# Kernel tuning notes

Measured on AMD Instinct MI355X. Metric: run time of the kernel, lower is better.

Reference implementation:

```python
import jax, jax.numpy as jnp
import numpy as np

B, C, H, W = 4, 128, 256, 256
HIDDEN = max(C // 8, 4)  # SE hidden


def haar_dwt(x):
    # x: (B,C,H,W), H,W even. Haar 2x2 stride-2 depthwise conv via block reshape.
    b_, c_, h_, w_ = x.shape
    xb = x.reshape(b_, c_, h_ // 2, 2, w_ // 2, 2)
    a = xb[:, :, :, 0, :, 0]
    b = xb[:, :, :, 0, :, 1]
    c = xb[:, :, :, 1, :, 0]
    d = xb[:, :, :, 1, :, 1]
    LL = 0.5 * (a + b + c + d)
    LH = 0.5 * (-a + b - c + d)
    HL = 0.5 * (-a - b + c + d)
    HH = 0.5 * (a - b - c + d)
    return LH, HL, HH, LL


def haar_idwt(LH, HL, HH, LL):
    # inverse of the depthwise conv_transpose with the same Haar kernels
    a = 0.5 * (LL - LH - HL + HH)
    b = 0.5 * (LL + LH - HL - HH)
    c = 0.5 * (LL - LH + HL - HH)
    d = 0.5 * (LL + LH + HL + HH)
    top = jnp.stack([a, b], axis=-1)      # (B,C,h,w,2)
    bot = jnp.stack([c, d], axis=-1)      # (B,C,h,w,2)
    blk = jnp.stack([top, bot], axis=-2)  # (B,C,h,w,2,2) -> rows x cols
    Bs, Cs, h, w = LL.shape
    return blk.transpose(0, 1, 2, 4, 3, 5).reshape(Bs, Cs, 2 * h, 2 * w)


def soft_threshold(x, thr):
    return jnp.sign(x) * jax.nn.relu(jnp.abs(x) - thr)


def setup_inputs() -> dict:
    key = jax.random.key(0)
    ks = jax.random.split(key, 9)
    x = jax.random.normal(ks[0], (B, C, H, W), dtype=jnp.float32)
    theta = jax.random.normal(ks[1], (3, C, 1, 1), dtype=jnp.float32) * 0.02
    dir_gate = jax.random.normal(ks[2], (3, C, 1, 1), dtype=jnp.float32) * 0.02
    fc_w = jax.random.normal(ks[3], (C, C), dtype=jnp.float32) * (1.0 / np.sqrt(C))
    fc_b = jax.random.normal(ks[4], (C,), dtype=jnp.float32) * 0.02
    sub_redistribute = jax.random.normal(ks[5], (C, 3), dtype=jnp.float32) * 0.02
    se_w1 = jax.random.normal(ks[6], (HIDDEN, C), dtype=jnp.float32) * (1.0 / np.sqrt(C))
    se_b1 = jnp.zeros((HIDDEN,), dtype=jnp.float32)
    se_w2 = jax.random.normal(ks[7], (C, HIDDEN), dtype=jnp.float32) * (1.0 / np.sqrt(HIDDEN))
    se_b2 = jnp.zeros((C,), dtype=jnp.float32)
    gamma = jnp.float32(0.5)
    return {"x": x, "theta": theta, "dir_gate": dir_gate, "fc_w": fc_w,
            "fc_b": fc_b, "sub_redistribute": sub_redistribute,
            "se_w1": se_w1, "se_b1": se_b1, "se_w2": se_w2, "se_b2": se_b2,
            "gamma": gamma}


def reference(x, theta, dir_gate, fc_w, fc_b, sub_redistribute,
              se_w1, se_b1, se_w2, se_b2, gamma):
    eps = 1e-6
    LH, HL, HH, LL = haar_dwt(x)

    # per-(B,C) abs-mean thresholds
    m_LH = jnp.mean(jnp.abs(LH), axis=(2, 3), keepdims=True) + eps
    m_HL = jnp.mean(jnp.abs(HL), axis=(2, 3), keepdims=True) + eps
    m_HH = jnp.mean(jnp.abs(HH), axis=(2, 3), keepdims=True) + eps
    t = jax.nn.sigmoid(theta)  # (3,C,1,1)
    LH_hat = soft_threshold(LH, t[0][None] * m_LH)
    HL_hat = soft_threshold(HL, t[1][None] * m_HL)
    HH_hat = soft_threshold(HH, t[2][None] * m_HH)

    g = jax.nn.sigmoid(dir_gate)
    LH_hat = LH_hat * g[0][None]
    HL_hat = HL_hat * g[1][None]
    HH_hat = HH_hat * g[2][None]

    stack3 = jnp.stack([LH_hat, HL_hat, HH_hat], axis=2)  # (B,C,3,h,w)
    attn_band = jax.nn.softmax(jnp.mean(jnp.abs(stack3), axis=1, keepdims=True), axis=2)
    H_mix = jnp.sum(stack3 * attn_band, axis=2)  # (B,C,h,w)

    w_redis = jax.nn.softmax(sub_redistribute, axis=1)  # (C,3)
    H_redist = H_mix[:, :, None] * w_redis[None, :, :, None, None]  # (B,C,3,h,w)
    X_re = haar_idwt(H_redist[:, :, 0], H_redist[:, :, 1], H_redist[:, :, 2], LL)

    # channel softmax gate from GAP + fc
    gap_vec = jnp.mean(X_re, axis=(2, 3))  # (B,C)
    gap_vec = gap_vec @ fc_w.T + fc_b
    w_softmax = jax.nn.softmax(gap_vec, axis=1)[:, :, None, None]

    # SE gate
    z = jnp.mean(X_re, axis=(2, 3))  # (B,C)
    z = jax.nn.relu(z @ se_w1.T + se_b1)
    w_se = jax.nn.sigmoid(z @ se_w2.T + se_b2)[:, :, None, None]

    return x * w_softmax + gamma * (X_re * w_se)
```

## Files before the change

### kernel.cpp

```cpp
#include <hip/hip_runtime.h>
#include <math.h>

#define BB 4
#define CC 128
#define HHH 256
#define WWW 256
#define HWSZ (HHH*WWW)
#define HIDDEN 16
#define NPAIR 8192
#define FCHUNK 16
#define NFCHUNK (NPAIR/FCHUNK)
#define RQUART 4

typedef float nfloat4 __attribute__((ext_vector_type(4)));

struct CParams {
    float thr0, thr1, thr2;
    float gA0, gA1, gA2;
    float gF0, gF1, gF2;
    float wsm, e0q;
    float ca, cb, cc, cd;
    float pad0;
};
static_assert(sizeof(CParams) == 64, "CParams must be 64B");

__device__ __forceinline__ float sigmoidf_(float v) { return 1.0f / (1.0f + expf(-v)); }

__global__ __launch_bounds__(256) void k_reduce(const float* __restrict__ x,
                                                float4* __restrict__ partial) {
    const int bq = blockIdx.x;
    const int bc = bq >> 2;
    const int quarter = bq & 3;
    const float* base = x + (size_t)bc * HWSZ;
    const int tid = threadIdx.x;
    float a0 = 0.f, a1 = 0.f, a2 = 0.f, sx = 0.f;
    #pragma unroll
    for (int i = 0; i < 8; ++i) {
        const int p = quarter * 2048 + i * 256 + tid;
        const int r = p >> 6;
        const int q = p & 63;
        const float4 t  = *(const float4*)(base + (2*r)   * WWW + 4*q);
        const float4 bo = *(const float4*)(base + (2*r+1) * WWW + 4*q);
        {   const float a = t.x, b_ = t.y, c_ = bo.x, d = bo.y;
            const float u1 = a + b_, u2 = c_ + d, u3 = a + c_, u4 = b_ + d, u5 = a + d, u6 = b_ + c_;
            a0 += fabsf(u4 - u3);
            a1 += fabsf(u2 - u1);
            a2 += fabsf(u5 - u6);
            sx += u1 + u2;
        }
        {   const float a = t.z, b_ = t.w, c_ = bo.z, d = bo.w;
            const float u1 = a + b_, u2 = c_ + d, u3 = a + c_, u4 = b_ + d, u5 = a + d, u6 = b_ + c_;
            a0 += fabsf(u4 - u3);
            a1 += fabsf(u2 - u1);
            a2 += fabsf(u5 - u6);
            sx += u1 + u2;
        }
    }
    __shared__ float4 red[256];
    red[tid] = make_float4(a0, a1, a2, sx);
    __syncthreads();
    for (int off = 128; off > 0; off >>= 1) {
        if (tid < off) {
            float4 o = red[tid + off];
            red[tid].x += o.x; red[tid].y += o.y; red[tid].z += o.z; red[tid].w += o.w;
        }
        __syncthreads();
    }
    if (tid == 0) partial[bq] = red[0];
}

__global__ __launch_bounds__(128) void k_params(
    const float4* __restrict__ partial,
    const float* __restrict__ theta, const float* __restrict__ dir_gate,
    const float* __restrict__ fc_w, const float* __restrict__ fc_b,
    const float* __restrict__ sub_r,
    const float* __restrict__ se_w1, const float* __restrict__ se_b1,
    const float* __restrict__ se_w2, const float* __restrict__ se_b2,
    const float* __restrict__ gamma_p,
    CParams* __restrict__ cbuf)
{
    const int b = blockIdx.x;
    const int i = threadIdx.x;
    __shared__ float gap[CC];
    __shared__ float z1[HIDDEN];
    __shared__ float red[CC];

    float4 s = make_float4(0.f, 0.f, 0.f, 0.f);
    #pragma unroll
    for (int k = 0; k < RQUART; ++k) {
        const float4 pq = partial[(b * CC + i) * RQUART + k];
        s.x += pq.x; s.y += pq.y; s.z += pq.z; s.w += pq.w;
    }
    gap[i] = s.w * (1.0f / 65536.0f);
    __syncthreads();

    float y = fc_b[i];
    for (int j = 0; j < CC; ++j) y += gap[j] * fc_w[i * CC + j];
    if (i < HIDDEN) {
        float z = se_b1[i];
        for (int j = 0; j < CC; ++j) z += gap[j] * se_w1[i * CC + j];
        z1[i] = fmaxf(z, 0.0f);
    }
    red[i] = y;
    __syncthreads();
    float mx = -1e30f;
    for (int j = 0; j < CC; ++j) mx = fmaxf(mx, red[j]);
    const float e = expf(y - mx);
    __syncthreads();
    red[i] = e;
    __syncthreads();
    float ssum = 0.f;
    for (int j = 0; j < CC; ++j) ssum += red[j];
    const float wsm = e / ssum;

    float wse = se_b2[i];
    for (int h = 0; h < HIDDEN; ++h) wse += z1[h] * se_w2[i * HIDDEN + h];
    wse = sigmoidf_(wse);
    const float wse2 = gamma_p[0] * wse;

    const float m0 = s.x * (0.5f / 16384.0f) + 1e-6f;
    const float m1 = s.y * (0.5f / 16384.0f) + 1e-6f;
    const float m2 = s.z * (0.5f / 16384.0f) + 1e-6f;
    CParams p;
    const float g0 = sigmoidf_(dir_gate[0 * CC + i]);
    const float g1 = sigmoidf_(dir_gate[1 * CC + i]);
    const float g2 = sigmoidf_(dir_gate[2 * CC + i]);
    p.thr0 = 2.0f * sigmoidf_(theta[0 * CC + i]) * m0;
    p.thr1 = 2.0f * sigmoidf_(theta[1 * CC + i]) * m1;
    p.thr2 = 2.0f * sigmoidf_(theta[2 * CC + i]) * m2;
    p.gA0 = g0; p.gA1 = g1; p.gA2 = g2;
    p.gF0 = 0.5f * g0 * wse2;
    p.gF1 = 0.5f * g1 * wse2;
    p.gF2 = 0.5f * g2 * wse2;
    p.wsm = wsm;
    p.e0q = 0.25f * wse2;
    const float r0 = sub_r[i * 3 + 0], r1 = sub_r[i * 3 + 1], r2 = sub_r[i * 3 + 2];
    const float rm = fmaxf(r0, fmaxf(r1, r2));
    const float e0 = expf(r0 - rm), e1 = expf(r1 - rm), e2 = expf(r2 - rm);
    const float inv = 1.0f / (e0 + e1 + e2);
    const float w0 = e0 * inv, w1 = e1 * inv, w2 = e2 * inv;
    p.ca = 0.5f * (-w0 - w1 + w2);
    p.cb = 0.5f * ( w0 - w1 - w2);
    p.cc = 0.5f * (-w0 + w1 - w2);
    p.cd = 0.5f * ( w0 + w1 + w2);
    p.pad0 = 0.f;
    cbuf[b * CC + i] = p;
}

__global__ __launch_bounds__(256) void k_fused(const float* __restrict__ x,
                                               const CParams* __restrict__ cbuf,
                                               float* __restrict__ out) {
    const int b = blockIdx.y;
    const int chunk = blockIdx.x;
    const int tid = threadIdx.x;
    const int pp = tid & 15;
    const int g  = tid >> 4;

    __shared__ CParams cp[CC];
    __shared__ float red2[16][16][6];
    __shared__ float att2[16][4];
    {
        const float* src = (const float*)(cbuf + b * CC);
        float* dst = (float*)cp;
        for (int i = tid; i < CC * 16; i += 256) dst[i] = src[i];
    }
    __syncthreads();

    const int p  = chunk * FCHUNK + pp;
    const int rp = p >> 6, q = p & 63;
    const float* base = x + (size_t)b * CC * HWSZ + (2*rp) * WWW + 4*q;

    float4 st[8], sb[8];
    float sA0=0, sA1=0, sA2=0, sB0=0, sB1=0, sB2=0;
    #pragma unroll
    for (int ci = 0; ci < 8; ++ci) {
        const int c = g * 8 + ci;
        const float* pc = base + c * HWSZ;
        st[ci] = *(const float4*)(pc);
        sb[ci] = *(const float4*)(pc + WWW);
        const float thr0 = cp[c].thr0, thr1 = cp[c].thr1, thr2 = cp[c].thr2;
        const float gA0 = cp[c].gA0, gA1 = cp[c].gA1, gA2 = cp[c].gA2;
        {   const float a = st[ci].x, b_ = st[ci].y, c_ = sb[ci].x, d = sb[ci].y;
            const float u1 = a + b_, u2 = c_ + d, u3 = a + c_, u4 = b_ + d, u5 = a + d, u6 = b_ + c_;
            sA0 += gA0 * fmaxf(fabsf(u4 - u3) - thr0, 0.f);
            sA1 += gA1 * fmaxf(fabsf(u2 - u1) - thr1, 0.f);
            sA2 += gA2 * fmaxf(fabsf(u5 - u6) - thr2, 0.f);
        }
        {   const float a = st[ci].z, b_ = st[ci].w, c_ = sb[ci].z, d = sb[ci].w;
            const float u1 = a + b_, u2 = c_ + d, u3 = a + c_, u4 = b_ + d, u5 = a + d, u6 = b_ + c_;
            sB0 += gA0 * fmaxf(fabsf(u4 - u3) - thr0, 0.f);
            sB1 += gA1 * fmaxf(fabsf(u2 - u1) - thr1, 0.f);
            sB2 += gA2 * fmaxf(fabsf(u5 - u6) - thr2, 0.f);
        }
    }
    red2[g][pp][0] = sA0; red2[g][pp][1] = sA1; red2[g][pp][2] = sA2;
    red2[g][pp][3] = sB0; red2[g][pp][4] = sB1; red2[g][pp][5] = sB2;
    __syncthreads();

    if (tid < 32) {
        const int pair = tid >> 1, h = tid & 1;
        float v0 = 0.f, v1 = 0.f, v2 = 0.f;
        #pragma unroll
        for (int gg = 0; gg < 16; ++gg) {
            v0 += red2[gg][pair][3*h + 0];
            v1 += red2[gg][pair][3*h + 1];
            v2 += red2[gg][pair][3*h + 2];
        }
        v0 *= (0.5f / CC); v1 *= (0.5f / CC); v2 *= (0.5f / CC);
        const float mx = fmaxf(v0, fmaxf(v1, v2));
        const float e0 = expf(v0 - mx), e1 = expf(v1 - mx), e2 = expf(v2 - mx);
        const float inv = 1.0f / (e0 + e1 + e2);
        att2[pair][2*h + 0] = e0 * inv;
        att2[pair][2*h + 1] = e1 * inv;
    }
    __syncthreads();

    const float a0A = att2[pp][0], a1A = att2[pp][1], a2A = 1.0f - a0A - a1A;
    const float a0B = att2[pp][2], a1B = att2[pp][3], a2B = 1.0f - a0B - a1B;

    float* obase = out + (size_t)b * CC * HWSZ + (2*rp) * WWW + 4*q;
    #pragma unroll
    for (int ci = 0; ci < 8; ++ci) {
        const int c = g * 8 + ci;
        const float thr0 = cp[c].thr0, thr1 = cp[c].thr1, thr2 = cp[c].thr2;
        const float gF0 = cp[c].gF0, gF1 = cp[c].gF1, gF2 = cp[c].gF2;
        const float wsm = cp[c].wsm, e0q = cp[c].e0q;
        const float ca = cp[c].ca, cb = cp[c].cb, ccc = cp[c].cc, cd = cp[c].cd;
        const float m0A = a0A * gF0, m1A = a1A * gF1, m2A = a2A * gF2;
        const float m0B = a0B * gF0, m1B = a1B * gF1, m2B = a2B * gF2;
        nfloat4 otop, obot;
        {   const float a = st[ci].x, b_ = st[ci].y, c_ = sb[ci].x, d = sb[ci].y;
            const float u1 = a + b_, u2 = c_ + d, u3 = a + c_, u4 = b_ + d, u5 = a + d, u6 = b_ + c_;
            const float B0 = u4 - u3, B1 = u2 - u1, B2 = u5 - u6;
            const float LL2 = u1 + u2;
            const float s0 = copysignf(fmaxf(fabsf(B0) - thr0, 0.f), B0);
            const float s1 = copysignf(fmaxf(fabsf(B1) - thr1, 0.f), B1);
            const float s2 = copysignf(fmaxf(fabsf(B2) - thr2, 0.f), B2);
            const float Hf = s0*m0A + s1*m1A + s2*m2A;
            const float T  = e0q * LL2;
            otop.x = fmaf(a , wsm, fmaf(Hf, ca , T));
            otop.y = fmaf(b_, wsm, fmaf(Hf, cb , T));
            obot.x = fmaf(c_, wsm, fmaf(Hf, ccc, T));
            obot.y = fmaf(d , wsm, fmaf(Hf, cd , T));
        }
        {   const float a = st[ci].z, b_ = st[ci].w, c_ = sb[ci].z, d = sb[ci].w;
            const float u1 = a + b_, u2 = c_ + d, u3 = a + c_, u4 = b_ + d, u5 = a + d, u6 = b_ + c_;
            const float B0 = u4 - u3, B1 = u2 - u1, B2 = u5 - u6;
            const float LL2 = u1 + u2;
            const float s0 = copysignf(fmaxf(fabsf(B0) - thr0, 0.f), B0);
            const float s1 = copysignf(fmaxf(fabsf(B1) - thr1, 0.f), B1);
            const float s2 = copysignf(fmaxf(fabsf(B2) - thr2, 0.f), B2);
            const float Hf = s0*m0B + s1*m1B + s2*m2B;
            const float T  = e0q * LL2;
            otop.z = fmaf(a , wsm, fmaf(Hf, ca , T));
            otop.w = fmaf(b_, wsm, fmaf(Hf, cb , T));
            obot.z = fmaf(c_, wsm, fmaf(Hf, ccc, T));
            obot.w = fmaf(d , wsm, fmaf(Hf, cd , T));
        }
        float* po = obase + c * HWSZ;
        __builtin_nontemporal_store(otop, (nfloat4*)(po));
        __builtin_nontemporal_store(obot, (nfloat4*)(po + WWW));
    }
}

extern "C" void kernel_launch(void* const* d_in, const int* in_sizes, int n_in,
                              void* d_out, int out_size, void* d_ws, size_t ws_size,
                              hipStream_t stream) {
    const float* x        = (const float*)d_in[0];
    const float* theta    = (const float*)d_in[1];
    const float* dir_gate = (const float*)d_in[2];
    const float* fc_w     = (const float*)d_in[3];
    const float* fc_b     = (const float*)d_in[4];
    const float* sub_r    = (const float*)d_in[5];
    const float* se_w1    = (const float*)d_in[6];
    const float* se_b1    = (const float*)d_in[7];
    const float* se_w2    = (const float*)d_in[8];
    const float* se_b2    = (const float*)d_in[9];
    const float* gamma_p  = (const float*)d_in[10];
    float* out = (float*)d_out;

    char* ws = (char*)d_ws;
    float4*  partial = (float4*)(ws);
    CParams* cbuf    = (CParams*)(ws + 32768);

    k_reduce<<<dim3(BB * CC * RQUART), dim3(256), 0, stream>>>(x, partial);
    k_params<<<dim3(BB), dim3(CC), 0, stream>>>(partial, theta, dir_gate, fc_w, fc_b,
                                                sub_r, se_w1, se_b1, se_w2, se_b2,
                                                gamma_p, cbuf);
    k_fused<<<dim3(NFCHUNK, BB), dim3(256), 0, stream>>>(x, cbuf, out);
}
```

Before: 75.36 us.

## Halve pixels per block, 4 channels per thread, pad channel params in LDS

The fused kernel now handles 8 pixel pairs per block instead of 16, with 32 channel groups of 4 channels each instead of 16 groups of 8. This halves the number of float4 values each thread keeps live across the band-attention reduction, which should lower register pressure and raise occupancy, and it doubles the grid size. The per-channel parameter table in shared memory is padded to a stride of 17 floats to avoid LDS bank conflicts. The cross-group reduction becomes a two-stage shared-memory reduction with an extra barrier. The cost is more blocks, each reloading the parameter table, and more reduction traffic.

```diff
diff --git a/kernel.cpp b/kernel.cpp
--- a/kernel.cpp
+++ b/kernel.cpp
@@ -8,9 +8,11 @@
 #define HWSZ (HHH*WWW)
 #define HIDDEN 16
 #define NPAIR 8192
-#define FCHUNK 16
-#define NFCHUNK (NPAIR/FCHUNK)
+#define FP 8
+#define NFCHUNK (NPAIR/FP)
+#define NG 32
 #define RQUART 4
+#define CPW 17
 
 typedef float nfloat4 __attribute__((ext_vector_type(4)));
 
@@ -153,33 +155,37 @@
     const int b = blockIdx.y;
     const int chunk = blockIdx.x;
     const int tid = threadIdx.x;
-    const int pp = tid & 15;
-    const int g  = tid >> 4;
-
-    __shared__ CParams cp[CC];
-    __shared__ float red2[16][16][6];
-    __shared__ float att2[16][4];
+    const int pp = tid & 7;
+    const int g  = tid >> 3;
+
+    __shared__ float cpa[CC * CPW];
+    __shared__ float red2[NG][FP][6];
+    __shared__ float vsum[FP][6];
+    __shared__ float att2[FP][4];
     {
         const float* src = (const float*)(cbuf + b * CC);
-        float* dst = (float*)cp;
-        for (int i = tid; i < CC * 16; i += 256) dst[i] = src[i];
-    }
-    __syncthreads();
-
-    const int p  = chunk * FCHUNK + pp;
+        for (int i = tid; i < CC * 16; i += 256) {
+            const int c = i >> 4, f = i & 15;
+            cpa[c * CPW + f] = src[i];
+        }
+    }
+    __syncthreads();
+
+    const int p  = chunk * FP + pp;
     const int rp = p >> 6, q = p & 63;
     const float* base = x + (size_t)b * CC * HWSZ + (2*rp) * WWW + 4*q;
 
-    float4 st[8], sb[8];
+    float4 st[4], sb[4];
     float sA0=0, sA1=0, sA2=0, sB0=0, sB1=0, sB2=0;
     #pragma unroll
-    for (int ci = 0; ci < 8; ++ci) {
-        const int c = g * 8 + ci;
+    for (int ci = 0; ci < 4; ++ci) {
+        const int c = g * 4 + ci;
         const float* pc = base + c * HWSZ;
         st[ci] = *(const float4*)(pc);
         sb[ci] = *(const float4*)(pc + WWW);
-        const float thr0 = cp[c].thr0, thr1 = cp[c].thr1, thr2 = cp[c].thr2;
-        const float gA0 = cp[c].gA0, gA1 = cp[c].gA1, gA2 = cp[c].gA2;
+        const float* cp = cpa + c * CPW;
+        const float thr0 = cp[0], thr1 = cp[1], thr2 = cp[2];
+        const float gA0 = cp[3], gA1 = cp[4], gA2 = cp[5];
         {   const float a = st[ci].x, b_ = st[ci].y, c_ = sb[ci].x, d = sb[ci].y;
             const float u1 = a + b_, u2 = c_ + d, u3 = a + c_, u4 = b_ + d, u5 = a + d, u6 = b_ + c_;
             sA0 += gA0 * fmaxf(fabsf(u4 - u3) - thr0, 0.f);
@@ -197,16 +203,19 @@
     red2[g][pp][3] = sB0; red2[g][pp][4] = sB1; red2[g][pp][5] = sB2;
     __syncthreads();
 
-    if (tid < 32) {
+    if (tid < FP * 6) {
+        const int pair = tid & 7, kk = tid >> 3;
+        float acc = 0.f;
+        #pragma unroll
+        for (int gg = 0; gg < NG; ++gg) acc += red2[gg][pair][kk];
+        vsum[pair][kk] = acc;
+    }
+    __syncthreads();
+    if (tid < FP * 2) {
         const int pair = tid >> 1, h = tid & 1;
-        float v0 = 0.f, v1 = 0.f, v2 = 0.f;
-        #pragma unroll
-        for (int gg = 0; gg < 16; ++gg) {
-            v0 += red2[gg][pair][3*h + 0];
-            v1 += red2[gg][pair][3*h + 1];
-            v2 += red2[gg][pair][3*h + 2];
-        }
-        v0 *= (0.5f / CC); v1 *= (0.5f / CC); v2 *= (0.5f / CC);
+        const float v0 = vsum[pair][3*h+0] * (0.5f / CC);
+        const float v1 = vsum[pair][3*h+1] * (0.5f / CC);
+        const float v2 = vsum[pair][3*h+2] * (0.5f / CC);
         const float mx = fmaxf(v0, fmaxf(v1, v2));
         const float e0 = expf(v0 - mx), e1 = expf(v1 - mx), e2 = expf(v2 - mx);
         const float inv = 1.0f / (e0 + e1 + e2);
@@ -220,12 +229,13 @@
 
     float* obase = out + (size_t)b * CC * HWSZ + (2*rp) * WWW + 4*q;
     #pragma unroll
-    for (int ci = 0; ci < 8; ++ci) {
-        const int c = g * 8 + ci;
-        const float thr0 = cp[c].thr0, thr1 = cp[c].thr1, thr2 = cp[c].thr2;
-        const float gF0 = cp[c].gF0, gF1 = cp[c].gF1, gF2 = cp[c].gF2;
-        const float wsm = cp[c].wsm, e0q = cp[c].e0q;
-        const float ca = cp[c].ca, cb = cp[c].cb, ccc = cp[c].cc, cd = cp[c].cd;
+    for (int ci = 0; ci < 4; ++ci) {
+        const int c = g * 4 + ci;
+        const float* cp = cpa + c * CPW;
+        const float thr0 = cp[0], thr1 = cp[1], thr2 = cp[2];
+        const float gF0 = cp[6], gF1 = cp[7], gF2 = cp[8];
+        const float wsm = cp[9], e0q = cp[10];
+        const float ca = cp[11], cb = cp[12], ccc = cp[13], cd = cp[14];
         const float m0A = a0A * gF0, m1A = a1A * gF1, m2A = a2A * gF2;
         const float m0B = a0B * gF0, m1B = a1B * gF1, m2B = a2B * gF2;
         nfloat4 otop, obot;
```

New measurement: 76.27 us. About the same (+1.2%).
